# Optimization experiments

Hardware: AMD Instinct MI355X
Metric: run time of the kernel (lower is better)

## Reference

```python
import jax, jax.numpy as jnp
import numpy as np

NHEAD = 8
ATTN_EPS = 1e-6
LN_EPS = 1e-5


def _layernorm(y, g, b):
    mu = jnp.mean(y, axis=-1, keepdims=True)
    var = jnp.var(y, axis=-1, keepdims=True)
    return (y - mu) * jax.lax.rsqrt(var + LN_EPS) * g + b


def setup_inputs() -> dict:
    key = jax.random.key(0)
    ks = jax.random.split(key, 6)
    B, L, D = 2, 8192, 1024
    s = 1.0 / np.sqrt(D)
    return {
        "x": jax.random.normal(ks[0], (B, L, D), jnp.float32),
        "Wq": jax.random.normal(ks[1], (D, D), jnp.float32) * s,
        "Wm": jax.random.normal(ks[2], (D, D), jnp.float32) * s,
        "W1": jax.random.normal(ks[3], (D, 2 * D), jnp.float32) * s,
        "W2": jax.random.normal(ks[4], (2 * D, D), jnp.float32) * (1.0 / np.sqrt(2 * D)),
        "g1": jnp.ones((D,), jnp.float32),
        "b1": jnp.zeros((D,), jnp.float32),
        "g2": jnp.ones((D,), jnp.float32),
        "b2": jnp.zeros((D,), jnp.float32),
    }


def reference(x, Wq, Wm, W1, W2, g1, b1, g2, b2):
    B, L, D = x.shape
    H = NHEAD
    d = D // H
    # NOTE: original forward uses q_proj for query, key AND value (faithful).
    q = (x @ Wq).reshape(B, L, H, d)  # [B,L,H,d]
    feat = jax.nn.elu(q) + 1.0        # elu feature map, shared by Q and K
    Q = feat
    K = feat
    V = q / L                          # value = value / v_length
    # KV outer-product sum over sequence: [B,H,d,d]
    KV = jnp.einsum('nshd,nshv->nhdv', K, V)
    # normalizer Z: [B,L,H]
    Ksum = K.sum(axis=1)               # [B,H,d]
    Z = 1.0 / (jnp.einsum('nlhd,nhd->nlh', Q, Ksum) + ATTN_EPS)
    msg = jnp.einsum('nlhd,nhdv,nlh->nlhv', Q, KV, Z) * L  # [B,L,H,d]
    msg = msg.reshape(B, L, D) @ Wm    # merge heads
    x = x + _layernorm(msg, g1, b1)
    # NOTE: MLP is applied to `message`, not the updated x (faithful to source).
    mlp = jax.nn.relu(msg @ W1) @ W2
    x = x + _layernorm(mlp, g2, b2)
    return x
```

## Files before the change

### kernel.cpp

```cpp
#include <hip/hip_runtime.h>
#include <hip/hip_bf16.h>
#include <stdint.h>

#define AS1 __attribute__((address_space(1)))
#define AS3 __attribute__((address_space(3)))

typedef __bf16 bf16x8 __attribute__((ext_vector_type(8)));
typedef __bf16 bf16x2 __attribute__((ext_vector_type(2)));
typedef float  f32x4  __attribute__((ext_vector_type(4)));

static constexpr int kL   = 8192;
static constexpr int kD   = 1024;
static constexpr int kM   = 2 * kL;
static constexpr int kNCH = 16;
static constexpr int kSCH = kL / kNCH;

__device__ __forceinline__ void async_cp16(__bf16* lds, const __bf16* g) {
    __builtin_amdgcn_global_load_lds((AS1 uint32_t*)g, (AS3 uint32_t*)lds, 16, 0, 0);
}

__device__ __forceinline__ float elu1f(float x) {
    return x > 0.0f ? x + 1.0f : __expf(x);
}

__device__ __forceinline__ bf16x8 elu8(bf16x8 v) {
    bf16x8 r;
#pragma unroll
    for (int j = 0; j < 8; ++j) r[j] = (__bf16)elu1f((float)v[j]);
    return r;
}

template <int M0>
__device__ __forceinline__ void mfma16(f32x4 (&acc)[8][4], const bf16x8 (&af)[4],
                                       const bf16x8 (&bq)[4]) {
#pragma unroll
    for (int i = 0; i < 4; ++i)
#pragma unroll
        for (int n = 0; n < 4; ++n)
            acc[M0 + i][n] = __builtin_amdgcn_mfma_f32_16x16x32_bf16(af[i], bq[n], acc[M0 + i][n], 0, 0, 0);
}

template <int EPI>
__global__ __launch_bounds__(512, 2) void gemm256(const __bf16* __restrict__ A,
                                                  const __bf16* __restrict__ Bt,
                                                  __bf16* __restrict__ C,
                                                  int M, int N, int K) {
    __shared__ __bf16 As[32768];
    __shared__ __bf16 Bs[32768];
    const int tid  = threadIdx.x;
    const int w    = tid >> 6;
    const int l    = tid & 63;
    const int quad = l >> 4;
    const int l16  = l & 15;
    const int wm   = w >> 2;
    const int wn   = w & 3;
    const int row0 = blockIdx.x * 256;
    const int col0 = blockIdx.y * 256;

    const int srow = l >> 2;
    const int sc   = ((l & 3) - (srow >> 1)) & 3;
    const __bf16* Ag0 = A  + (size_t)(row0 + w * 32 + srow) * K + sc * 8;
    const __bf16* Bg0 = Bt + (size_t)(col0 + w * 32 + srow) * K + sc * 8;
    const size_t r16K = (size_t)16 * K;
    const int NT = K >> 6;

    const int fpos = ((quad + (l16 >> 1)) & 3) * 8;
    const int arow = wm * 4096 + l16 * 32 + fpos;
    const int brow = wn * 2048 + l16 * 32 + fpos;

    f32x4 acc[8][4] = {};

    auto stage_h = [&](int ts, int hh) {
        if (ts >= NT) return;
        const int off = (ts & 1) * 16384 + (hh >> 1) * 8192 + w * 1024;
        const int ko  = ts * 64 + (hh >> 1) * 32;
        if ((hh & 1) == 0) {
            async_cp16(&As[off], Ag0 + ko);
            async_cp16(&As[off + 512], Ag0 + ko + r16K);
        } else {
            async_cp16(&Bs[off], Bg0 + ko);
            async_cp16(&Bs[off + 512], Bg0 + ko + r16K);
        }
    };

    stage_h(0, 0); stage_h(0, 1); stage_h(0, 2); stage_h(0, 3);
    asm volatile("s_waitcnt vmcnt(4)" ::: "memory");
    stage_h(1, 0); stage_h(1, 1); stage_h(1, 2);
    asm volatile("s_waitcnt vmcnt(6)" ::: "memory");
    __builtin_amdgcn_s_barrier();

    for (int t = 0; t < NT; ++t) {
        const int bo = (t & 1) * 16384;
        bf16x8 af[4], bq[4];

#pragma unroll
        for (int i = 0; i < 4; ++i) af[i] = *(const bf16x8*)&As[bo + arow + i * 512];
#pragma unroll
        for (int n = 0; n < 4; ++n) bq[n] = *(const bf16x8*)&Bs[bo + brow + n * 512];
        stage_h(t + 1, 3);
        __builtin_amdgcn_s_barrier();
        asm volatile("s_waitcnt lgkmcnt(0)" ::: "memory");
        __builtin_amdgcn_sched_barrier(0);
        __builtin_amdgcn_s_setprio(1);
        mfma16<0>(acc, af, bq);
        __builtin_amdgcn_s_setprio(0);
        __builtin_amdgcn_s_barrier();

#pragma unroll
        for (int i = 0; i < 4; ++i) af[i] = *(const bf16x8*)&As[bo + arow + 2048 + i * 512];
        stage_h(t + 2, 0);
        __builtin_amdgcn_s_barrier();
        asm volatile("s_waitcnt lgkmcnt(0)" ::: "memory");
        __builtin_amdgcn_sched_barrier(0);
        __builtin_amdgcn_s_setprio(1);
        mfma16<4>(acc, af, bq);
        __builtin_amdgcn_s_setprio(0);
        __builtin_amdgcn_s_barrier();

#pragma unroll
        for (int i = 0; i < 4; ++i) af[i] = *(const bf16x8*)&As[bo + 8192 + arow + i * 512];
#pragma unroll
        for (int n = 0; n < 4; ++n) bq[n] = *(const bf16x8*)&Bs[bo + 8192 + brow + n * 512];
        stage_h(t + 2, 1);
        __builtin_amdgcn_s_barrier();
        asm volatile("s_waitcnt lgkmcnt(0)" ::: "memory");
        __builtin_amdgcn_sched_barrier(0);
        __builtin_amdgcn_s_setprio(1);
        mfma16<0>(acc, af, bq);
        __builtin_amdgcn_s_setprio(0);
        __builtin_amdgcn_s_barrier();

#pragma unroll
        for (int i = 0; i < 4; ++i) af[i] = *(const bf16x8*)&As[bo + 8192 + arow + 2048 + i * 512];
        stage_h(t + 2, 2);
        __builtin_amdgcn_s_barrier();
        asm volatile("s_waitcnt lgkmcnt(0)" ::: "memory");
        __builtin_amdgcn_sched_barrier(0);
        __builtin_amdgcn_s_setprio(1);
        mfma16<4>(acc, af, bq);
        __builtin_amdgcn_s_setprio(0);
        if (t + 2 < NT)       { asm volatile("s_waitcnt vmcnt(6)" ::: "memory"); }
        else if (t + 2 == NT) { asm volatile("s_waitcnt vmcnt(0)" ::: "memory"); }
        __builtin_amdgcn_s_barrier();
    }

#pragma unroll
    for (int m = 0; m < 8; ++m) {
        const int rowb = row0 + wm * 128 + m * 16 + quad * 4;
#pragma unroll
        for (int n = 0; n < 4; ++n) {
            const int col = col0 + wn * 64 + n * 16 + l16;
#pragma unroll
            for (int r = 0; r < 4; ++r) {
                float v = acc[m][n][r];
                if (EPI == 1) v = v > 0.0f ? v : 0.0f;
                C[(size_t)(rowb + r) * N + col] = (__bf16)v;
            }
        }
    }
    (void)M;
}

__device__ __forceinline__ void transpose_body(const float* __restrict__ in,
                                               __bf16* __restrict__ out,
                                               int R, int Ccols, int bx, int by,
                                               int t, __bf16 (*tile)[33]) {
    const int bc = bx * 32, br = by * 32;
    const int tx = t & 31, ty = t >> 5;
#pragma unroll
    for (int i = ty; i < 32; i += 8)
        tile[i][tx] = (__bf16)in[(size_t)(br + i) * Ccols + bc + tx];
    __syncthreads();
#pragma unroll
    for (int i = ty; i < 32; i += 8)
        out[(size_t)(bc + i) * R + br + tx] = tile[tx][i];
}

__global__ __launch_bounds__(256) void prep(const float* __restrict__ x,
                                            __bf16* __restrict__ xb,
                                            const float* __restrict__ Wq,
                                            __bf16* __restrict__ WqT,
                                            const float* __restrict__ Wm,
                                            __bf16* __restrict__ WmT,
                                            const float* __restrict__ W1,
                                            __bf16* __restrict__ W1T,
                                            const float* __restrict__ W2,
                                            __bf16* __restrict__ W2T) {
    __shared__ __bf16 tile[32][33];
    const int t = threadIdx.x;
    int id = blockIdx.x;
    if (id < 8192) {
        const size_t i = ((size_t)id * 256 + t) * 8;
        f32x4 a = *(const f32x4*)(x + i);
        f32x4 b = *(const f32x4*)(x + i + 4);
        bf16x8 o;
#pragma unroll
        for (int j = 0; j < 4; ++j) { o[j] = (__bf16)a[j]; o[4 + j] = (__bf16)b[j]; }
        *(bf16x8*)(xb + i) = o;
        return;
    }
    id -= 8192;
    if (id < 1024) {
        transpose_body(Wq, WqT, 1024, 1024, id & 31, id >> 5, t, tile);
    } else if (id < 2048) {
        const int i2 = id - 1024;
        transpose_body(Wm, WmT, 1024, 1024, i2 & 31, i2 >> 5, t, tile);
    } else if (id < 4096) {
        const int i2 = id - 2048;
        transpose_body(W1, W1T, 1024, 2048, i2 & 63, i2 >> 6, t, tile);
    } else {
        const int i2 = id - 4096;
        transpose_body(W2, W2T, 2048, 1024, i2 & 31, i2 >> 5, t, tile);
    }
}

__global__ __launch_bounds__(256) void transpose_q(const __bf16* __restrict__ q,
                                                   __bf16* __restrict__ qT) {
    __shared__ __bf16 qs[64 * 130];
    const int bh = blockIdx.x, b = bh >> 3, h = bh & 7;
    const int s0 = blockIdx.y * 64;
    const int t = threadIdx.x;
    const size_t rowbase = (size_t)b * 8388608 + (size_t)h * 128;

#pragma unroll
    for (int c = 0; c < 4; ++c) {
        const int id = c * 256 + t;
        const int r = id >> 4, col = (id & 15) * 8;
        bf16x8 qv = *(const bf16x8*)(q + rowbase + (size_t)(s0 + r) * 1024 + col);
        const int lb = r * 130 + col;
#pragma unroll
        for (int p = 0; p < 4; ++p) {
            bf16x2 qp = { qv[2 * p], qv[2 * p + 1] };
            *(bf16x2*)&qs[lb + 2 * p] = qp;
        }
    }
    __syncthreads();

    const size_t ob = (size_t)bh * (128 * 8192) + s0;
#pragma unroll
    for (int c = 0; c < 4; ++c) {
        const int id = c * 256 + t;
        const int dk = id >> 3, sch = id & 7;
        bf16x8 ov;
#pragma unroll
        for (int j = 0; j < 8; ++j) ov[j] = qs[(sch * 8 + j) * 130 + dk];
        *(bf16x8*)(qT + ob + (size_t)dk * 8192 + sch * 8) = ov;
    }
}

__global__ __launch_bounds__(256) void kv_gemm(const __bf16* __restrict__ qT,
                                               float* __restrict__ KVpart,
                                               float* __restrict__ Kspart) {
    __shared__ __bf16 Qs[2][128 * 32];
    const int tid  = threadIdx.x;
    const int wave = tid >> 6, lane = tid & 63;
    const int quad = lane >> 4, l16 = lane & 15;
    const int wm = wave & 1, wn = wave >> 1;
    const int bh = blockIdx.x, ch = blockIdx.y;

    f32x4 acc[4][4] = {};
    float ksacc[4] = {};

    const int srow = lane >> 2;
    const int sk8  = ((lane & 3) - (srow >> 1)) & 3;
    const size_t base = (size_t)bh * (128 * 8192) + ch * kSCH + sk8 * 8;
    const __bf16* Qg0 = qT + base + (size_t)(wave * 32 + srow) * 8192;
    const size_t r16 = (size_t)16 * 8192;
    const int ldsw = wave * 1024;
    const int fp = ((quad + (l16 >> 1)) & 3) * 8;
    const int frow = l16 * 32 + fp;
    const int nk = kSCH / 32;
    {
        async_cp16(&Qs[0][ldsw], Qg0);
        async_cp16(&Qs[0][ldsw + 512], Qg0 + r16);
    }
    for (int k = 0; k < nk; ++k) {
        __syncthreads();
        if (k + 1 < nk) {
            const int nb = (k + 1) & 1;
            const int ko = (k + 1) << 5;
            async_cp16(&Qs[nb][ldsw], Qg0 + ko);
            async_cp16(&Qs[nb][ldsw + 512], Qg0 + r16 + ko);
        }
        const __bf16* Qsb = Qs[k & 1];
        bf16x8 af[4], bfr[4];
#pragma unroll
        for (int i = 0; i < 4; ++i)
            af[i] = elu8(*(const bf16x8*)&Qsb[(wm * 4 + i) * 512 + frow]);
#pragma unroll
        for (int j = 0; j < 4; ++j)
            bfr[j] = *(const bf16x8*)&Qsb[(wn * 4 + j) * 512 + frow];
        if (wn == 0) {
#pragma unroll
            for (int i = 0; i < 4; ++i)
#pragma unroll
                for (int j = 0; j < 8; ++j) ksacc[i] += (float)af[i][j];
        }
#pragma unroll
        for (int i = 0; i < 4; ++i)
#pragma unroll
            for (int j = 0; j < 4; ++j)
                acc[i][j] = __builtin_amdgcn_mfma_f32_16x16x32_bf16(af[i], bfr[j], acc[i][j], 0, 0, 0);
    }

    float* outp = KVpart + (((size_t)bh * kNCH + ch) << 14);
#pragma unroll
    for (int i = 0; i < 4; ++i) {
        const int rowb = wm * 64 + i * 16 + quad * 4;
#pragma unroll
        for (int j = 0; j < 4; ++j) {
            const int col = wn * 64 + j * 16 + l16;
#pragma unroll
            for (int r = 0; r < 4; ++r)
                outp[(rowb + r) * 128 + col] = acc[i][j][r];
        }
    }
    if (wn == 0) {
#pragma unroll
        for (int i = 0; i < 4; ++i) {
            float v = ksacc[i];
            v += __shfl_xor(v, 16);
            v += __shfl_xor(v, 32);
            if (quad == 0)
                Kspart[((size_t)bh * kNCH + ch) * 128 + wm * 64 + i * 16 + l16] = v;
        }
    }
}

__global__ __launch_bounds__(256) void reduce_kv(const float* __restrict__ KVpart,
                                                 const float* __restrict__ Kspart,
                                                 __bf16* __restrict__ KVbT,
                                                 float* __restrict__ Ksum) {
    const int t = threadIdx.x;
    if (blockIdx.x < 1024) {
        const size_t o = (size_t)blockIdx.x * 256 + t;
        const size_t bh = o >> 14;
        const size_t rem = o & 16383;
        float s = 0.f;
#pragma unroll 4
        for (int ch = 0; ch < kNCH; ++ch)
            s += KVpart[((bh * kNCH + ch) << 14) + rem];
        const int dk = (int)(rem >> 7), dv = (int)(rem & 127);
        KVbT[(bh << 14) + dv * 128 + dk] = (__bf16)s;
    } else {
        const int o = (blockIdx.x - 1024) * 256 + t;
        const int bh = o >> 7;
        const int dk = o & 127;
        float s = 0.f;
#pragma unroll 4
        for (int ch = 0; ch < kNCH; ++ch)
            s += Kspart[(bh * kNCH + ch) * 128 + dk];
        Ksum[o] = s;
    }
}

__global__ __launch_bounds__(256) void msg_gemm(const __bf16* __restrict__ q,
                                                const __bf16* __restrict__ KVbT,
                                                const float* __restrict__ Ks,
                                                __bf16* __restrict__ msg) {
    __shared__ __bf16 As[2][128 * 32];
    __shared__ __bf16 Bs[2][128 * 32];
    __shared__ float KsS[128];
    __shared__ float Zsh[128];
    const int tid  = threadIdx.x;
    const int wave = tid >> 6, lane = tid & 63;
    const int quad = lane >> 4, l16 = lane & 15;
    const int wm = wave & 1, wn = wave >> 1;
    const int bh = blockIdx.x, b = bh >> 3, h = bh & 7;
    const int row0 = blockIdx.y * 128;

    if (tid < 32)
        *(f32x4*)&KsS[tid * 4] = *(const f32x4*)(Ks + bh * 128 + tid * 4);

    f32x4 acc[4][4] = {};
    float zacc[4] = {};
    const int srow = lane >> 2;
    const int sk8  = ((lane & 3) - (srow >> 1)) & 3;
    const __bf16* Ag0 = q + (size_t)b * 8388608 + (size_t)(row0 + wave * 32 + srow) * 1024 + h * 128 + sk8 * 8;
    const __bf16* Bg0 = KVbT + ((size_t)bh << 14) + (wave * 32 + srow) * 128 + sk8 * 8;
    const size_t rA16 = (size_t)16 * 1024;
    const size_t rB16 = (size_t)16 * 128;
    const int ldsw = wave * 1024;
    const int fp = ((quad + (l16 >> 1)) & 3) * 8;
    const int frow = l16 * 32 + fp;
    const int nk = 4;
    {
        async_cp16(&As[0][ldsw], Ag0);
        async_cp16(&As[0][ldsw + 512], Ag0 + rA16);
        async_cp16(&Bs[0][ldsw], Bg0);
        async_cp16(&Bs[0][ldsw + 512], Bg0 + rB16);
    }
    for (int k = 0; k < nk; ++k) {
        __syncthreads();
        if (k + 1 < nk) {
            const int nb = (k + 1) & 1;
            const int ko = (k + 1) << 5;
            async_cp16(&As[nb][ldsw], Ag0 + ko);
            async_cp16(&As[nb][ldsw + 512], Ag0 + rA16 + ko);
            async_cp16(&Bs[nb][ldsw], Bg0 + ko);
            async_cp16(&Bs[nb][ldsw + 512], Bg0 + rB16 + ko);
        }
        const __bf16* Asb = As[k & 1];
        const __bf16* Bsb = Bs[k & 1];
        bf16x8 af[4], bfr[4];
#pragma unroll
        for (int i = 0; i < 4; ++i)
            af[i] = elu8(*(const bf16x8*)&Asb[(wm * 4 + i) * 512 + frow]);
#pragma unroll
        for (int j = 0; j < 4; ++j)
            bfr[j] = *(const bf16x8*)&Bsb[(wn * 4 + j) * 512 + frow];
        {
            f32x4 k0 = *(const f32x4*)&KsS[k * 32 + quad * 8];
            f32x4 k1 = *(const f32x4*)&KsS[k * 32 + quad * 8 + 4];
#pragma unroll
            for (int i = 0; i < 4; ++i) {
#pragma unroll
                for (int j = 0; j < 4; ++j) {
                    zacc[i] += (float)af[i][j] * k0[j];
                    zacc[i] += (float)af[i][4 + j] * k1[j];
                }
            }
        }
#pragma unroll
        for (int i = 0; i < 4; ++i)
#pragma unroll
            for (int j = 0; j < 4; ++j)
                acc[i][j] = __builtin_amdgcn_mfma_f32_16x16x32_bf16(af[i], bfr[j], acc[i][j], 0, 0, 0);
    }

#pragma unroll
    for (int i = 0; i < 4; ++i) {
        float v = zacc[i];
        v += __shfl_xor(v, 16);
        v += __shfl_xor(v, 32);
        if (wn == 0 && quad == 0)
            Zsh[wm * 64 + i * 16 + l16] = 1.0f / (v + 1e-6f);
    }
    __syncthreads();

    const size_t obase = (size_t)b * 8388608 + (size_t)h * 128;
#pragma unroll
    for (int i = 0; i < 4; ++i) {
        const int lr0 = wm * 64 + i * 16 + quad * 4;
#pragma unroll
        for (int j = 0; j < 4; ++j) {
            const int col = wn * 64 + j * 16 + l16;
#pragma unroll
            for (int r = 0; r < 4; ++r) {
                const float v = acc[i][j][r] * Zsh[lr0 + r];
                msg[obase + (size_t)(row0 + lr0 + r) * 1024 + col] = (__bf16)v;
            }
        }
    }
}

template <int BF16BASE>
__global__ __launch_bounds__(256) void ln_res(const void* __restrict__ basep,
                                              const __bf16* __restrict__ y,
                                              const float* __restrict__ g,
                                              const float* __restrict__ bvec,
                                              float* __restrict__ out) {
    const int wave = threadIdx.x >> 6, lane = threadIdx.x & 63;
    const int row = blockIdx.x * 4 + wave;
    const size_t ro = (size_t)row * kD + lane * 16;
    bf16x8 y0 = *(const bf16x8*)(y + ro);
    bf16x8 y1 = *(const bf16x8*)(y + ro + 8);
    float v[16];
    float s = 0.f, sq = 0.f;
#pragma unroll
    for (int j = 0; j < 8; ++j) { v[j] = (float)y0[j]; v[8 + j] = (float)y1[j]; }
#pragma unroll
    for (int j = 0; j < 16; ++j) { s += v[j]; sq += v[j] * v[j]; }
#pragma unroll
    for (int m = 1; m < 64; m <<= 1) { s += __shfl_xor(s, m); sq += __shfl_xor(sq, m); }
    const float mu = s * (1.0f / 1024.0f);
    float var = sq * (1.0f / 1024.0f) - mu * mu;
    if (var < 0.f) var = 0.f;
    const float rstd = rsqrtf(var + 1e-5f);
    const int go = lane * 16;
    float bs[16];
    if (BF16BASE) {
        bf16x8 b0 = *(const bf16x8*)((const __bf16*)basep + ro);
        bf16x8 b1 = *(const bf16x8*)((const __bf16*)basep + ro + 8);
#pragma unroll
        for (int j = 0; j < 8; ++j) { bs[j] = (float)b0[j]; bs[8 + j] = (float)b1[j]; }
    } else {
#pragma unroll
        for (int j = 0; j < 4; ++j) {
            f32x4 bb = *(const f32x4*)((const float*)basep + ro + j * 4);
#pragma unroll
            for (int r = 0; r < 4; ++r) bs[j * 4 + r] = bb[r];
        }
    }
#pragma unroll
    for (int j = 0; j < 4; ++j) {
        f32x4 gg = *(const f32x4*)(g + go + j * 4);
        f32x4 be = *(const f32x4*)(bvec + go + j * 4);
        f32x4 o;
#pragma unroll
        for (int r = 0; r < 4; ++r)
            o[r] = bs[j * 4 + r] + (v[j * 4 + r] - mu) * rstd * gg[r] + be[r];
        *(f32x4*)(out + ro + j * 4) = o;
    }
}

extern "C" void kernel_launch(void* const* d_in, const int* in_sizes, int n_in,
                              void* d_out, int out_size, void* d_ws, size_t ws_size,
                              hipStream_t stream) {
    const float* x  = (const float*)d_in[0];
    const float* Wq = (const float*)d_in[1];
    const float* Wm = (const float*)d_in[2];
    const float* W1 = (const float*)d_in[3];
    const float* W2 = (const float*)d_in[4];
    const float* g1 = (const float*)d_in[5];
    const float* b1 = (const float*)d_in[6];
    const float* g2 = (const float*)d_in[7];
    const float* b2 = (const float*)d_in[8];
    float* out = (float*)d_out;

    const size_t BLD = (size_t)kM * kD;
    __bf16* q    = (__bf16*)d_ws;
    __bf16* msg  = q + BLD;
    __bf16* hbuf = msg + BLD;
    __bf16* WqT  = hbuf + 2 * BLD;
    __bf16* WmT  = WqT + 1048576;
    __bf16* W1T  = WmT + 1048576;
    __bf16* W2T  = W1T + 2097152;
    __bf16* KVb  = W2T + 2097152;
    float* KVpart = (float*)(KVb + 262144);
    float* Kspart = KVpart + (size_t)kNCH * 16 * 16384;
    float* Ksum   = Kspart + (size_t)16 * kNCH * 128;
    const size_t need = ((char*)(Ksum + 2048)) - (char*)d_ws;
    if (ws_size < need) return;

    __bf16* xb   = hbuf;
    __bf16* qT   = hbuf + BLD;
    __bf16* msg2 = q;
    __bf16* mlp  = msg;

    const dim3 blk(256);
    const dim3 blk5(512);

    prep<<<dim3(14336), blk, 0, stream>>>(x, xb, Wq, WqT, Wm, WmT, W1, W1T, W2, W2T);

    gemm256<0><<<dim3(kM / 256, kD / 256), blk5, 0, stream>>>(xb, WqT, q, kM, kD, kD);
    transpose_q<<<dim3(16, 128), blk, 0, stream>>>(q, qT);
    kv_gemm<<<dim3(16, kNCH), blk, 0, stream>>>(qT, KVpart, Kspart);
    reduce_kv<<<dim3(1032), blk, 0, stream>>>(KVpart, Kspart, KVb, Ksum);
    msg_gemm<<<dim3(16, kL / 128), blk, 0, stream>>>(q, KVb, Ksum, msg);
    gemm256<0><<<dim3(kM / 256, kD / 256), blk5, 0, stream>>>(msg, WmT, msg2, kM, kD, kD);
    ln_res<1><<<dim3(kM / 4), blk, 0, stream>>>(xb, msg2, g1, b1, out);
    gemm256<1><<<dim3(kM / 256, 2048 / 256), blk5, 0, stream>>>(msg2, W1T, hbuf, kM, 2048, kD);
    gemm256<0><<<dim3(kM / 256, kD / 256), blk5, 0, stream>>>(hbuf, W2T, mlp, kM, kD, 2048);
    ln_res<0><<<dim3(kM / 4), blk, 0, stream>>>(out, mlp, g2, b2, out);
    (void)in_sizes; (void)n_in; (void)out_size;
}
```

Baseline: 450.3 us.

## Pre-swizzle KV into LDS-ready layout and load whole KV tile once in msg_gemm

reduce_kv now sums the KV partials with vectorized loads, transposes through shared memory and writes KV in the exact swizzled chunk layout msg_gemm uses in LDS. msg_gemm loads the full 128x128 KV block for its head into LDS once at the start, so only the Q tile remains double-buffered through the k loop. The intent is to remove the strided scalar transpose writes in reduce_kv and the repeated per-step KV staging in msg_gemm. In exchange reduce_kv runs only 64 KV blocks, which limits its parallelism, and msg_gemm uses more LDS per block, which may lower occupancy.

```diff
diff --git a/kernel.cpp b/kernel.cpp
--- a/kernel.cpp
+++ b/kernel.cpp
@@ -329,21 +329,51 @@
 
 __global__ __launch_bounds__(256) void reduce_kv(const float* __restrict__ KVpart,
                                                  const float* __restrict__ Kspart,
-                                                 __bf16* __restrict__ KVbT,
+                                                 __bf16* __restrict__ KVswz,
                                                  float* __restrict__ Ksum) {
     const int t = threadIdx.x;
-    if (blockIdx.x < 1024) {
-        const size_t o = (size_t)blockIdx.x * 256 + t;
-        const size_t bh = o >> 14;
-        const size_t rem = o & 16383;
-        float s = 0.f;
-#pragma unroll 4
-        for (int ch = 0; ch < kNCH; ++ch)
-            s += KVpart[((bh * kNCH + ch) << 14) + rem];
-        const int dk = (int)(rem >> 7), dv = (int)(rem & 127);
-        KVbT[(bh << 14) + dv * 128 + dk] = (__bf16)s;
+    if (blockIdx.x < 64) {
+        __shared__ float T[128][33];
+        const int bh = blockIdx.x >> 2;
+        const int ks = blockIdx.x & 3;
+        const int dk0 = ks * 32;
+        const size_t base0 = ((size_t)bh * kNCH) << 14;
+
+        f32x4 acc[4] = {};
+#pragma unroll 2
+        for (int ch = 0; ch < kNCH; ++ch) {
+            const float* p = KVpart + base0 + ((size_t)ch << 14) + dk0 * 128;
+#pragma unroll
+            for (int i = 0; i < 4; ++i) {
+                f32x4 v = *(const f32x4*)(p + (size_t)(t + i * 256) * 4);
+#pragma unroll
+                for (int j = 0; j < 4; ++j) acc[i][j] += v[j];
+            }
+        }
+#pragma unroll
+        for (int i = 0; i < 4; ++i) {
+            const int f0 = (t + i * 256) * 4;
+#pragma unroll
+            for (int j = 0; j < 4; ++j) {
+                const int f = f0 + j;
+                T[f & 127][f >> 7] = acc[i][j];
+            }
+        }
+        __syncthreads();
+        const int dv = t >> 1;
+        const int half = t & 1;
+        __bf16* outb = KVswz + ((size_t)bh << 14) + ks * 4096 + dv * 32;
+#pragma unroll
+        for (int gg = 0; gg < 2; ++gg) {
+            const int g = half * 2 + gg;
+            const int c = (g + (dv >> 1)) & 3;
+            bf16x8 o;
+#pragma unroll
+            for (int j = 0; j < 8; ++j) o[j] = (__bf16)T[dv][g * 8 + j];
+            *(bf16x8*)(outb + c * 8) = o;
+        }
     } else {
-        const int o = (blockIdx.x - 1024) * 256 + t;
+        const int o = (blockIdx.x - 64) * 256 + t;
         const int bh = o >> 7;
         const int dk = o & 127;
         float s = 0.f;
@@ -355,11 +385,11 @@
 }
 
 __global__ __launch_bounds__(256) void msg_gemm(const __bf16* __restrict__ q,
-                                                const __bf16* __restrict__ KVbT,
+                                                const __bf16* __restrict__ KVswz,
                                                 const float* __restrict__ Ks,
                                                 __bf16* __restrict__ msg) {
-    __shared__ __bf16 As[2][128 * 32];
-    __shared__ __bf16 Bs[2][128 * 32];
+    __shared__ __bf16 As2[2][4096];
+    __shared__ __bf16 Bsf[16384];
     __shared__ float KsS[128];
     __shared__ float Zsh[128];
     const int tid  = threadIdx.x;
@@ -377,31 +407,29 @@
     const int srow = lane >> 2;
     const int sk8  = ((lane & 3) - (srow >> 1)) & 3;
     const __bf16* Ag0 = q + (size_t)b * 8388608 + (size_t)(row0 + wave * 32 + srow) * 1024 + h * 128 + sk8 * 8;
-    const __bf16* Bg0 = KVbT + ((size_t)bh << 14) + (wave * 32 + srow) * 128 + sk8 * 8;
     const size_t rA16 = (size_t)16 * 1024;
-    const size_t rB16 = (size_t)16 * 128;
     const int ldsw = wave * 1024;
     const int fp = ((quad + (l16 >> 1)) & 3) * 8;
     const int frow = l16 * 32 + fp;
     const int nk = 4;
     {
-        async_cp16(&As[0][ldsw], Ag0);
-        async_cp16(&As[0][ldsw + 512], Ag0 + rA16);
-        async_cp16(&Bs[0][ldsw], Bg0);
-        async_cp16(&Bs[0][ldsw + 512], Bg0 + rB16);
+        const __bf16* bg = KVswz + ((size_t)bh << 14);
+#pragma unroll
+        for (int c = 0; c < 8; ++c)
+            async_cp16(&Bsf[(c * 256 + tid) * 8 - lane * 8 + lane * 8], bg + (c * 256 + tid) * 8);
+        async_cp16(&As2[0][ldsw], Ag0);
+        async_cp16(&As2[0][ldsw + 512], Ag0 + rA16);
     }
     for (int k = 0; k < nk; ++k) {
         __syncthreads();
         if (k + 1 < nk) {
             const int nb = (k + 1) & 1;
             const int ko = (k + 1) << 5;
-            async_cp16(&As[nb][ldsw], Ag0 + ko);
-            async_cp16(&As[nb][ldsw + 512], Ag0 + rA16 + ko);
-            async_cp16(&Bs[nb][ldsw], Bg0 + ko);
-            async_cp16(&Bs[nb][ldsw + 512], Bg0 + rB16 + ko);
-        }
-        const __bf16* Asb = As[k & 1];
-        const __bf16* Bsb = Bs[k & 1];
+            async_cp16(&As2[nb][ldsw], Ag0 + ko);
+            async_cp16(&As2[nb][ldsw + 512], Ag0 + rA16 + ko);
+        }
+        const __bf16* Asb = As2[k & 1];
+        const __bf16* Bsb = &Bsf[k * 4096];
         bf16x8 af[4], bfr[4];
 #pragma unroll
         for (int i = 0; i < 4; ++i)
@@ -546,7 +574,7 @@
     gemm256<0><<<dim3(kM / 256, kD / 256), blk5, 0, stream>>>(xb, WqT, q, kM, kD, kD);
     transpose_q<<<dim3(16, 128), blk, 0, stream>>>(q, qT);
     kv_gemm<<<dim3(16, kNCH), blk, 0, stream>>>(qT, KVpart, Kspart);
-    reduce_kv<<<dim3(1032), blk, 0, stream>>>(KVpart, Kspart, KVb, Ksum);
+    reduce_kv<<<dim3(72), blk, 0, stream>>>(KVpart, Kspart, KVb, Ksum);
     msg_gemm<<<dim3(16, kL / 128), blk, 0, stream>>>(q, KVb, Ksum, msg);
     gemm256<0><<<dim3(kM / 256, kD / 256), blk5, 0, stream>>>(msg, WmT, msg2, kM, kD, kD);
     ln_res<1><<<dim3(kM / 4), blk, 0, stream>>>(xb, msg2, g1, b1, out);
```

Result: no change. 456.9 us (+1.5%).

## Fuse q transpose into projection GEMM epilogue and vectorize KV reduction

Applied to the files above, without the earlier changes.

The Q-projection GEMM gets a new epilogue mode that stages the bf16 tile through the now-idle shared-memory buffers using an XOR swizzle. It then writes the per-head transposed layout directly, so the separate transpose_q kernel and its re-read of q are removed. The KV partial reduction now loads four floats per thread and launches a quarter as many blocks. The trade-off is an extra LDS round-trip and two barriers at the end of that GEMM, and the KV reduction's transposed stores stay scattered.

```diff
diff --git a/kernel.cpp b/kernel.cpp
--- a/kernel.cpp
+++ b/kernel.cpp
@@ -6,7 +6,7 @@
 #define AS3 __attribute__((address_space(3)))
 
 typedef __bf16 bf16x8 __attribute__((ext_vector_type(8)));
-typedef __bf16 bf16x2 __attribute__((ext_vector_type(2)));
+typedef __bf16 bf16x4 __attribute__((ext_vector_type(4)));
 typedef float  f32x4  __attribute__((ext_vector_type(4)));
 
 static constexpr int kL   = 8192;
@@ -44,6 +44,7 @@
 __global__ __launch_bounds__(512, 2) void gemm256(const __bf16* __restrict__ A,
                                                   const __bf16* __restrict__ Bt,
                                                   __bf16* __restrict__ C,
+                                                  __bf16* __restrict__ qTp,
                                                   int M, int N, int K) {
     __shared__ __bf16 As[32768];
     __shared__ __bf16 Bs[32768];
@@ -156,6 +157,40 @@
                 if (EPI == 1) v = v > 0.0f ? v : 0.0f;
                 C[(size_t)(rowb + r) * N + col] = (__bf16)v;
             }
+        }
+    }
+
+    if (EPI == 2) {
+        __builtin_amdgcn_s_barrier();
+        {
+            __bf16* dst = (wn >> 1) ? Bs : As;
+#pragma unroll
+            for (int m = 0; m < 8; ++m) {
+                const int soff = wm * 128 + m * 16 + quad * 4;
+#pragma unroll
+                for (int n = 0; n < 4; ++n) {
+                    const int dk = (wn & 1) * 64 + n * 16 + l16;
+                    bf16x4 v4;
+#pragma unroll
+                    for (int r = 0; r < 4; ++r) v4[r] = (__bf16)acc[m][n][r];
+                    *(bf16x4*)&dst[dk * 256 + (soff ^ ((dk & 7) << 3))] = v4;
+                }
+            }
+        }
+        __builtin_amdgcn_s_barrier();
+        const int bb = row0 >> 13;
+        const int s0 = row0 & 8191;
+#pragma unroll
+        for (int c = 0; c < 16; ++c) {
+            const int idx = c * 512 + tid;
+            const int hh  = idx >> 12;
+            const int dkl = (idx >> 5) & 127;
+            const int scc = (idx & 31) * 8;
+            const __bf16* src = hh ? Bs : As;
+            bf16x8 v = *(const bf16x8*)&src[dkl * 256 + (scc ^ ((dkl & 7) << 3))];
+            const int hglob = (col0 >> 7) + hh;
+            *(bf16x8*)(qTp + (((size_t)(bb * 8 + hglob)) << 20) +
+                       ((size_t)dkl << 13) + s0 + scc) = v;
         }
     }
     (void)M;
@@ -214,40 +249,6 @@
     }
 }
 
-__global__ __launch_bounds__(256) void transpose_q(const __bf16* __restrict__ q,
-                                                   __bf16* __restrict__ qT) {
-    __shared__ __bf16 qs[64 * 130];
-    const int bh = blockIdx.x, b = bh >> 3, h = bh & 7;
-    const int s0 = blockIdx.y * 64;
-    const int t = threadIdx.x;
-    const size_t rowbase = (size_t)b * 8388608 + (size_t)h * 128;
-
-#pragma unroll
-    for (int c = 0; c < 4; ++c) {
-        const int id = c * 256 + t;
-        const int r = id >> 4, col = (id & 15) * 8;
-        bf16x8 qv = *(const bf16x8*)(q + rowbase + (size_t)(s0 + r) * 1024 + col);
-        const int lb = r * 130 + col;
-#pragma unroll
-        for (int p = 0; p < 4; ++p) {
-            bf16x2 qp = { qv[2 * p], qv[2 * p + 1] };
-            *(bf16x2*)&qs[lb + 2 * p] = qp;
-        }
-    }
-    __syncthreads();
-
-    const size_t ob = (size_t)bh * (128 * 8192) + s0;
-#pragma unroll
-    for (int c = 0; c < 4; ++c) {
-        const int id = c * 256 + t;
-        const int dk = id >> 3, sch = id & 7;
-        bf16x8 ov;
-#pragma unroll
-        for (int j = 0; j < 8; ++j) ov[j] = qs[(sch * 8 + j) * 130 + dk];
-        *(bf16x8*)(qT + ob + (size_t)dk * 8192 + sch * 8) = ov;
-    }
-}
-
 __global__ __launch_bounds__(256) void kv_gemm(const __bf16* __restrict__ qT,
                                                float* __restrict__ KVpart,
                                                float* __restrict__ Kspart) {
@@ -332,18 +333,23 @@
                                                  __bf16* __restrict__ KVbT,
                                                  float* __restrict__ Ksum) {
     const int t = threadIdx.x;
-    if (blockIdx.x < 1024) {
-        const size_t o = (size_t)blockIdx.x * 256 + t;
-        const size_t bh = o >> 14;
-        const size_t rem = o & 16383;
-        float s = 0.f;
+    if (blockIdx.x < 256) {
+        const size_t o4 = ((size_t)blockIdx.x * 256 + t) * 4;
+        const size_t bh = o4 >> 14;
+        const size_t rem = o4 & 16383;
+        f32x4 s = {};
 #pragma unroll 4
-        for (int ch = 0; ch < kNCH; ++ch)
-            s += KVpart[((bh * kNCH + ch) << 14) + rem];
-        const int dk = (int)(rem >> 7), dv = (int)(rem & 127);
-        KVbT[(bh << 14) + dv * 128 + dk] = (__bf16)s;
+        for (int ch = 0; ch < kNCH; ++ch) {
+            f32x4 v = *(const f32x4*)&KVpart[((bh * kNCH + ch) << 14) + rem];
+#pragma unroll
+            for (int j = 0; j < 4; ++j) s[j] += v[j];
+        }
+        const int dk = (int)(rem >> 7), dv0 = (int)(rem & 127);
+#pragma unroll
+        for (int j = 0; j < 4; ++j)
+            KVbT[(bh << 14) + (dv0 + j) * 128 + dk] = (__bf16)s[j];
     } else {
-        const int o = (blockIdx.x - 1024) * 256 + t;
+        const int o = (blockIdx.x - 256) * 256 + t;
         const int bh = o >> 7;
         const int dk = o & 127;
         float s = 0.f;
@@ -543,15 +549,14 @@
 
     prep<<<dim3(14336), blk, 0, stream>>>(x, xb, Wq, WqT, Wm, WmT, W1, W1T, W2, W2T);
 
-    gemm256<0><<<dim3(kM / 256, kD / 256), blk5, 0, stream>>>(xb, WqT, q, kM, kD, kD);
-    transpose_q<<<dim3(16, 128), blk, 0, stream>>>(q, qT);
+    gemm256<2><<<dim3(kM / 256, kD / 256), blk5, 0, stream>>>(xb, WqT, q, qT, kM, kD, kD);
     kv_gemm<<<dim3(16, kNCH), blk, 0, stream>>>(qT, KVpart, Kspart);
-    reduce_kv<<<dim3(1032), blk, 0, stream>>>(KVpart, Kspart, KVb, Ksum);
+    reduce_kv<<<dim3(264), blk, 0, stream>>>(KVpart, Kspart, KVb, Ksum);
     msg_gemm<<<dim3(16, kL / 128), blk, 0, stream>>>(q, KVb, Ksum, msg);
-    gemm256<0><<<dim3(kM / 256, kD / 256), blk5, 0, stream>>>(msg, WmT, msg2, kM, kD, kD);
+    gemm256<0><<<dim3(kM / 256, kD / 256), blk5, 0, stream>>>(msg, WmT, msg2, nullptr, kM, kD, kD);
     ln_res<1><<<dim3(kM / 4), blk, 0, stream>>>(xb, msg2, g1, b1, out);
-    gemm256<1><<<dim3(kM / 256, 2048 / 256), blk5, 0, stream>>>(msg2, W1T, hbuf, kM, 2048, kD);
-    gemm256<0><<<dim3(kM / 256, kD / 256), blk5, 0, stream>>>(hbuf, W2T, mlp, kM, kD, 2048);
+    gemm256<1><<<dim3(kM / 256, 2048 / 256), blk5, 0, stream>>>(msg2, W1T, hbuf, nullptr, kM, 2048, kD);
+    gemm256<0><<<dim3(kM / 256, kD / 256), blk5, 0, stream>>>(hbuf, W2T, mlp, nullptr, kM, kD, 2048);
     ln_res<0><<<dim3(kM / 4), blk, 0, stream>>>(out, mlp, g2, b2, out);
     (void)in_sizes; (void)n_in; (void)out_size;
 }
```

Result: no change. 454.2 us (+0.9%).
